# Optimization experiments

Measured on AMD Instinct MI355X. Metric: run time of the kernel, lower is better.

## Reference

```python
import jax, jax.numpy as jnp
import numpy as np
import math

NH, NKV, D = 32, 8, 128  # heads, kv heads, head dim

def _alibi_slopes(n):
    cp2 = 2 ** math.floor(math.log2(n))
    base = 2.0 ** (-8.0 / cp2)
    slopes = base ** np.arange(1, cp2 + 1, dtype=np.float32)
    if cp2 != n:
        extra_base = 2.0 ** (-4.0 / cp2)
        extra = extra_base ** np.arange(1, 1 + 2 * (n - cp2), 2, dtype=np.float32)
        slopes = np.concatenate([slopes, extra])
    return slopes.astype(np.float32)

def setup_inputs() -> dict:
    key = jax.random.key(0)
    k1, k2, k3 = jax.random.split(key, 3)
    B, S, H = 4, 1024, 4096
    qkv_out = NH * D + 2 * NKV * D  # 6144
    return {
        "hidden_states": jax.random.normal(k1, (B, S, H), jnp.float32) * 0.02,
        "w_qkv": jax.random.normal(k2, (H, qkv_out), jnp.float32) * 0.02,
        "w_o": jax.random.normal(k3, (NH * D, H), jnp.float32) * 0.02,
    }

def reference(hidden_states, w_qkv, w_o):
    B, S, H = hidden_states.shape
    G = NH // NKV  # query groups per kv head
    scale = D ** -0.5

    qkv = hidden_states @ w_qkv  # [B,S,6144]
    q = qkv[..., : NH * D].reshape(B, S, NKV, G, D)
    k = qkv[..., NH * D : NH * D + NKV * D].reshape(B, S, NKV, D)
    v = qkv[..., NH * D + NKV * D :].reshape(B, S, NKV, D)

    scores = jnp.einsum("bqhgd,bkhd->bhgqk", q, k) * scale  # [B,NKV,G,S,S]

    slopes = jnp.asarray(_alibi_slopes(NH)).reshape(NKV, G)  # head order
    pos = jnp.arange(S)
    rel = pos[:, None] - pos[None, :]  # i - j
    sqrt_dist = jnp.sqrt(jnp.maximum(rel, 0).astype(jnp.float32))
    bias = -slopes[:, :, None, None] * sqrt_dist  # ALiBi-sqrt bias
    bias = jnp.where(rel[None, None] >= 0, bias, -jnp.inf)  # causal mask

    attn = jax.nn.softmax(scores + bias[None], axis=-1)
    out = jnp.einsum("bhgqk,bkhd->bqhgd", attn, v).reshape(B, S, NH * D)
    return out @ w_o
```

## Files before the change

kernel.cpp:

```cpp
#include <hip/hip_runtime.h>
#include <stdint.h>

typedef __attribute__((ext_vector_type(4))) float floatx4;
typedef __attribute__((ext_vector_type(8))) short short8;
typedef unsigned short ushort_t;

#define DEVI __device__ __forceinline__

constexpr int Bc   = 4;
constexpr int Sc   = 1024;
constexpr int Hc   = 4096;
constexpr int NHc  = 32;
constexpr int NKVc = 8;
constexpr int Dc   = 128;
constexpr int QKVO = 6144;
constexpr int Mc   = Bc * Sc;

DEVI ushort_t f2bf(float f) {
  union { float f; unsigned u; } x; x.f = f;
  unsigned u = x.u;
  u += 0x7fffu + ((u >> 16) & 1u);
  return (ushort_t)(u >> 16);
}

DEVI short8 cvt8(floatx4 a, floatx4 b) {
  short8 r;
  r[0] = (short)f2bf(a[0]); r[1] = (short)f2bf(a[1]);
  r[2] = (short)f2bf(a[2]); r[3] = (short)f2bf(a[3]);
  r[4] = (short)f2bf(b[0]); r[5] = (short)f2bf(b[1]);
  r[6] = (short)f2bf(b[2]); r[7] = (short)f2bf(b[3]);
  return r;
}

DEVI void load_lds16(const ushort_t* g, ushort_t* l) {
  __builtin_amdgcn_global_load_lds(
      (const __attribute__((address_space(1))) void*)g,
      (__attribute__((address_space(3))) void*)l, 16, 0, 0);
}

#define BARRIER()  asm volatile("s_barrier" ::: "memory")
#define LGKM0()    asm volatile("s_waitcnt lgkmcnt(0)" ::: "memory")
#define VMCNT(n)   asm volatile("s_waitcnt vmcnt(" #n ")" ::: "memory")

__global__ __launch_bounds__(256)
void cvt_bf16(const float* __restrict__ src, ushort_t* __restrict__ dst, int n8)
{
  const int i = blockIdx.x * 256 + threadIdx.x;
  if (i >= n8) return;
  const floatx4 f0 = *(const floatx4*)(src + (size_t)i * 8);
  const floatx4 f1 = *(const floatx4*)(src + (size_t)i * 8 + 4);
  *(short8*)(dst + (size_t)i * 8) = cvt8(f0, f1);
}

__global__ __launch_bounds__(256)
void transpose_cvt(const float* __restrict__ src, ushort_t* __restrict__ dst,
                   int R, int C)
{
  __shared__ float ts[64][67];
  const int cb = C >> 6;
  const int r0 = (blockIdx.x / cb) << 6;
  const int c0 = (blockIdx.x % cb) << 6;
  const int t  = threadIdx.x;

  const int lr = t >> 4, lc = (t & 15) << 2;
#pragma unroll
  for (int i = 0; i < 4; ++i) {
    const floatx4 v = *(const floatx4*)(src + (size_t)(r0 + lr + 16 * i) * C + c0 + lc);
#pragma unroll
    for (int j = 0; j < 4; ++j) ts[lr + 16 * i][lc + j] = v[j];
  }
  __syncthreads();

  const int c     = ((t >> 6) << 4) + ((t & 63) >> 2);
  const int chunk = t & 3;
  short8 t0, t1;
#pragma unroll
  for (int k = 0; k < 8; ++k) t0[k] = (short)f2bf(ts[chunk * 16 + k][c]);
#pragma unroll
  for (int k = 0; k < 8; ++k) t1[k] = (short)f2bf(ts[chunk * 16 + 8 + k][c]);
  ushort_t* dp = dst + (size_t)(c0 + c) * R + r0 + chunk * 16;
  *(short8*)dp       = t0;
  *(short8*)(dp + 8) = t1;
}

__global__ __launch_bounds__(256)
void v_transpose(const ushort_t* __restrict__ qkv, ushort_t* __restrict__ vt)
{
  __shared__ ushort_t ts[64][72];
  const int bid = blockIdx.x;
  const int db  = bid & 1;
  const int sb  = (bid >> 1) & 15;
  const int hkv = (bid >> 5) & 7;
  const int b   = bid >> 8;
  const int t   = threadIdx.x;

  const ushort_t* src = qkv + (size_t)(b * Sc + sb * 64) * QKVO
                        + (NHc * Dc + NKVc * Dc) + hkv * Dc + db * 64;
  const int lr = t >> 3, lc = (t & 7) * 8;
  *(short8*)&ts[lr][lc]      = *(const short8*)(src + (size_t)lr * QKVO + lc);
  *(short8*)&ts[lr + 32][lc] = *(const short8*)(src + (size_t)(lr + 32) * QKVO + lc);
  __syncthreads();

  ushort_t* dst = vt + ((size_t)(b * NKVc + hkv) * Dc + db * 64) * Sc + sb * 64;
  const int dr  = t >> 2;
  const int sc0 = (t & 3) * 16;
  short8 o0, o1;
#pragma unroll
  for (int k = 0; k < 8; ++k) o0[k] = (short)ts[sc0 + k][dr];
#pragma unroll
  for (int k = 0; k < 8; ++k) o1[k] = (short)ts[sc0 + 8 + k][dr];
  *(short8*)(dst + (size_t)dr * Sc + sc0)     = o0;
  *(short8*)(dst + (size_t)dr * Sc + sc0 + 8) = o1;
}

template<int NFRAG, bool OBF16>
__global__ __launch_bounds__(512, 2)
void gemm_nt8d(const ushort_t* __restrict__ A, const ushort_t* __restrict__ BT,
               void* __restrict__ Cp, int M, int N, int K)
{
  constexpr int BN = 64 * NFRAG;
  __shared__ __align__(16) ushort_t As[2][256 * 64];
  __shared__ __align__(16) ushort_t Bs[2][BN * 64];

  const int nb  = N / BN;
  const int nwg = (M >> 8) * nb;
  int bid = blockIdx.x;
  bid = (bid & 7) * (nwg >> 3) + (bid >> 3);
  const int bm = bid / nb, bn = bid % nb;
  const int m0 = bm << 8, n0 = bn * BN;

  const int tid  = threadIdx.x;
  const int wid  = tid >> 6, lane = tid & 63;
  const int wm   = wid >> 2, wn = wid & 3;
  const int fr   = lane & 15;
  const int g16  = (lane >> 4) << 4;
  const int rsw  = (fr & 7) << 4;
  const int l8   = lane >> 3;
  const int scol = ((lane & 7) ^ l8) << 3;

  const int sr   = (wid << 3);
  const size_t Ks = (size_t)K;
  const ushort_t* agS = A  + (size_t)(m0 + sr + l8) * K + scol;
  const ushort_t* bgS = BT + (size_t)(n0 + sr + l8) * K + scol;

  const int rowA = (wm * 128 + fr) * 128;
  const int rowB = (wn * 16 * NFRAG + fr) * 128;
  const int cb0  = g16 ^ rsw;
  const int cb1  = (64 + g16) ^ rsw;

  const floatx4 fz = {0.f, 0.f, 0.f, 0.f};
  floatx4 acc[8][NFRAG];
#pragma unroll
  for (int i = 0; i < 8; ++i)
#pragma unroll
    for (int f = 0; f < NFRAG; ++f) acc[i][f] = fz;

  auto SAq0 = [&](int s, size_t kn) {
    load_lds16(agS + kn,            &As[s][(sr +   0) * 64]);
    load_lds16(agS + 128 * Ks + kn, &As[s][(sr + 128) * 64]);
  };
  auto SAq1 = [&](int s, size_t kn) {
    load_lds16(agS +  64 * Ks + kn, &As[s][(sr +  64) * 64]);
    load_lds16(agS + 192 * Ks + kn, &As[s][(sr + 192) * 64]);
  };
  auto SB01 = [&](int s, size_t kn) {
    load_lds16(bgS + kn,            &Bs[s][(sr +   0) * 64]);
    load_lds16(bgS +  64 * Ks + kn, &Bs[s][(sr +  64) * 64]);
  };
  auto SB2 = [&](int s, size_t kn) {
    load_lds16(bgS + 128 * Ks + kn, &Bs[s][(sr + 128) * 64]);
    if constexpr (NFRAG == 4)
      load_lds16(bgS + 192 * Ks + kn, &Bs[s][(sr + 192) * 64]);
  };

  SAq0(0, 0); SAq1(0, 0); SB01(0, 0); SB2(0, 0);
  SAq0(1, 64); SB01(1, 64); SB2(1, 64);
  VMCNT(0);
  BARRIER();

#define LDA(s, i, ks) (*(const short8*)((const char*)&As[s][0] + rowA + (i) * 2048 + ((ks) ? cb1 : cb0)))
#define LDB(s, f, ks) (*(const short8*)((const char*)&Bs[s][0] + rowB + (f) * 2048 + ((ks) ? cb1 : cb0)))

  const int NI = K >> 7;
  for (int it = 0; it < NI; ++it) {
    const size_t kt0 = (size_t)it << 7;
    const size_t k1 = kt0 + 64, k2 = kt0 + 128, k3 = kt0 + 192;
    const bool st2 = (it + 1 < NI);
    const bool st3 = st2;

    short8 aR[4], bR[NFRAG][2], bS[NFRAG][2];

#define MFMA_PH(base, barr, ks)                                              \
    __builtin_amdgcn_s_setprio(1);                                          \
    _Pragma("unroll")                                                       \
    for (int i = 0; i < 4; ++i)                                             \
      _Pragma("unroll")                                                     \
      for (int f = 0; f < NFRAG; ++f)                                       \
        acc[(base) + i][f] = __builtin_amdgcn_mfma_f32_16x16x32_bf16(       \
            aR[i], barr[f][ks], acc[(base) + i][f], 0, 0, 0);               \
    __builtin_amdgcn_s_setprio(0);

#pragma unroll
    for (int i = 0; i < 4; ++i) aR[i] = LDA(0, i, 0);
#pragma unroll
    for (int f = 0; f < NFRAG; ++f) { bR[f][0] = LDB(0, f, 0); bR[f][1] = LDB(0, f, 1); }
    SAq1(1, k1);
    VMCNT(4);
    BARRIER();
    LGKM0(); __builtin_amdgcn_sched_barrier(0);
    MFMA_PH(0, bR, 0)
    BARRIER();

#pragma unroll
    for (int i = 0; i < 4; ++i) aR[i] = LDA(1, i, 0);
#pragma unroll
    for (int f = 0; f < NFRAG; ++f) { bS[f][0] = LDB(1, f, 0); bS[f][1] = LDB(1, f, 1); }
    if (st2) SB01(0, k2);
    VMCNT(4);
    BARRIER();
    LGKM0(); __builtin_amdgcn_sched_barrier(0);
    MFMA_PH(0, bS, 0)
    BARRIER();

#pragma unroll
    for (int i = 0; i < 4; ++i) aR[i] = LDA(0, 4 + i, 0);
    if (st2) SB2(0, k2);
    if constexpr (NFRAG == 4) { VMCNT(4); } else { VMCNT(3); }
    BARRIER();
    LGKM0(); __builtin_amdgcn_sched_barrier(0);
    MFMA_PH(4, bR, 0)
    BARRIER();

#pragma unroll
    for (int i = 0; i < 4; ++i) aR[i] = LDA(1, 4 + i, 0);
    if (st3) SB01(1, k3);
    BARRIER();
    LGKM0(); __builtin_amdgcn_sched_barrier(0);
    MFMA_PH(4, bS, 0)
    BARRIER();

#pragma unroll
    for (int i = 0; i < 4; ++i) aR[i] = LDA(0, i, 1);
    if (st3) SB2(1, k3);
    BARRIER();
    LGKM0(); __builtin_amdgcn_sched_barrier(0);
    MFMA_PH(0, bR, 1)
    BARRIER();

#pragma unroll
    for (int i = 0; i < 4; ++i) aR[i] = LDA(1, i, 1);
    if (st2) SAq0(0, k2);
    BARRIER();
    LGKM0(); __builtin_amdgcn_sched_barrier(0);
    MFMA_PH(0, bS, 1)
    BARRIER();

#pragma unroll
    for (int i = 0; i < 4; ++i) aR[i] = LDA(0, 4 + i, 1);
    if (st3) SAq0(1, k3);
    BARRIER();
    LGKM0(); __builtin_amdgcn_sched_barrier(0);
    MFMA_PH(4, bR, 1)
    BARRIER();

#pragma unroll
    for (int i = 0; i < 4; ++i) aR[i] = LDA(1, 4 + i, 1);
    if (st2) SAq1(0, k2);
    VMCNT(4);
    BARRIER();
    LGKM0(); __builtin_amdgcn_sched_barrier(0);
    MFMA_PH(4, bS, 1)
    BARRIER();

#undef MFMA_PH
  }
#undef LDA
#undef LDB

  const int r4 = (lane >> 4) << 2;
#pragma unroll
  for (int i = 0; i < 8; ++i) {
#pragma unroll
    for (int rr = 0; rr < 4; ++rr) {
      const size_t row = (size_t)(m0 + wm * 128 + i * 16 + r4 + rr);
#pragma unroll
      for (int f = 0; f < NFRAG; ++f) {
        const size_t col = (size_t)(n0 + wn * 16 * NFRAG + f * 16 + fr);
        if constexpr (OBF16)
          ((ushort_t*)Cp)[row * N + col] = f2bf(acc[i][f][rr]);
        else
          ((float*)Cp)[row * N + col] = acc[i][f][rr];
      }
    }
  }
}

template<int NFRAG, bool OBF16>
__global__ __launch_bounds__(512, 2)
void gemm_nt8s(const ushort_t* __restrict__ A, const ushort_t* __restrict__ BT,
               void* __restrict__ Cp, int M, int N, int K)
{
  constexpr int BN = 64 * NFRAG;
  __shared__ __align__(16) ushort_t As[2][256 * 64];
  __shared__ __align__(16) ushort_t Bs[2][BN * 64];

  const int nb  = N / BN;
  const int nwg = (M >> 8) * nb;
  int bid = blockIdx.x;
  bid = (bid & 7) * (nwg >> 3) + (bid >> 3);
  const int bm = bid / nb, bn = bid % nb;
  const int m0 = bm << 8, n0 = bn * BN;

  const int tid  = threadIdx.x;
  const int wid  = tid >> 6, lane = tid & 63;
  const int wm   = wid >> 2, wn = wid & 3;
  const int fr   = lane & 15;
  const int g16  = (lane >> 4) << 4;
  const int rsw  = (fr & 7) << 4;
  const int l8   = lane >> 3;
  const int scol = ((lane & 7) ^ l8) << 3;

  const int sr   = (wid << 3);
  const size_t Ks = (size_t)K;
  const ushort_t* agS = A  + (size_t)(m0 + sr + l8) * K + scol;
  const ushort_t* bgS = BT + (size_t)(n0 + sr + l8) * K + scol;

  const int rowA = (wm * 128 + fr) * 128;
  const int rowB = (wn * 16 * NFRAG + fr) * 128;
  const int cb0  = g16 ^ rsw;
  const int cb1  = (64 + g16) ^ rsw;

  const floatx4 fz = {0.f, 0.f, 0.f, 0.f};
  floatx4 acc[8][NFRAG];
#pragma unroll
  for (int i = 0; i < 8; ++i)
#pragma unroll
    for (int f = 0; f < NFRAG; ++f) acc[i][f] = fz;

  auto SAq0 = [&](int s, size_t kn) {
    load_lds16(agS + kn,            &As[s][(sr +   0) * 64]);
    load_lds16(agS + 128 * Ks + kn, &As[s][(sr + 128) * 64]);
  };
  auto SAq1 = [&](int s, size_t kn) {
    load_lds16(agS +  64 * Ks + kn, &As[s][(sr +  64) * 64]);
    load_lds16(agS + 192 * Ks + kn, &As[s][(sr + 192) * 64]);
  };
  auto SB01 = [&](int s, size_t kn) {
    load_lds16(bgS + kn,            &Bs[s][(sr +   0) * 64]);
    load_lds16(bgS +  64 * Ks + kn, &Bs[s][(sr +  64) * 64]);
  };
  auto SB2 = [&](int s, size_t kn) {
    load_lds16(bgS + 128 * Ks + kn, &Bs[s][(sr + 128) * 64]);
    if constexpr (NFRAG == 4)
      load_lds16(bgS + 192 * Ks + kn, &Bs[s][(sr + 192) * 64]);
  };

  SAq0(0, 0); SAq1(0, 0); SB01(0, 0); SB2(0, 0);
  SB01(1, 64); SB2(1, 64);
  VMCNT(4);
  BARRIER();

#define LDA(s, i, ks) (*(const short8*)((const char*)&As[s][0] + rowA + (i) * 2048 + ((ks) ? cb1 : cb0)))
#define LDB(s, f, ks) (*(const short8*)((const char*)&Bs[s][0] + rowB + (f) * 2048 + ((ks) ? cb1 : cb0)))

  const int NI = K >> 7;
  for (int it = 0; it < NI; ++it) {
    const size_t kt0 = (size_t)it << 7;
    const size_t k1 = kt0 + 64, k2 = kt0 + 128, k3 = kt0 + 192;
    const bool st = (it + 1 < NI);

    short8 aR[4], bR[NFRAG][2];

#define MFMA_PH(base, ks)                                                    \
    __builtin_amdgcn_s_setprio(1);                                          \
    _Pragma("unroll")                                                       \
    for (int i = 0; i < 4; ++i)                                             \
      _Pragma("unroll")                                                     \
      for (int f = 0; f < NFRAG; ++f)                                       \
        acc[(base) + i][f] = __builtin_amdgcn_mfma_f32_16x16x32_bf16(       \
            aR[i], bR[f][ks], acc[(base) + i][f], 0, 0, 0);                 \
    __builtin_amdgcn_s_setprio(0);

#pragma unroll
    for (int i = 0; i < 4; ++i) aR[i] = LDA(0, i, 0);
#pragma unroll
    for (int f = 0; f < NFRAG; ++f) { bR[f][0] = LDB(0, f, 0); bR[f][1] = LDB(0, f, 1); }
    SAq0(1, k1);
    BARRIER();
    LGKM0(); __builtin_amdgcn_sched_barrier(0);
    MFMA_PH(0, 0)
    BARRIER();

#pragma unroll
    for (int i = 0; i < 4; ++i) aR[i] = LDA(0, 4 + i, 0);
    SAq1(1, k1);
    BARRIER();
    LGKM0(); __builtin_amdgcn_sched_barrier(0);
    MFMA_PH(4, 0)
    BARRIER();

#pragma unroll
    for (int i = 0; i < 4; ++i) aR[i] = LDA(0, i, 1);
    if (st) SB01(0, k2);
    BARRIER();
    LGKM0(); __builtin_amdgcn_sched_barrier(0);
    MFMA_PH(0, 1)
    BARRIER();

#pragma unroll
    for (int i = 0; i < 4; ++i) aR[i] = LDA(0, 4 + i, 1);
    if (st) { SB2(0, k2); VMCNT(4); } else { VMCNT(0); }
    BARRIER();
    LGKM0(); __builtin_amdgcn_sched_barrier(0);
    MFMA_PH(4, 1)
    BARRIER();

#pragma unroll
    for (int i = 0; i < 4; ++i) aR[i] = LDA(1, i, 0);
#pragma unroll
    for (int f = 0; f < NFRAG; ++f) { bR[f][0] = LDB(1, f, 0); bR[f][1] = LDB(1, f, 1); }
    if (st) SAq0(0, k2);
    BARRIER();
    LGKM0(); __builtin_amdgcn_sched_barrier(0);
    MFMA_PH(0, 0)
    BARRIER();

#pragma unroll
    for (int i = 0; i < 4; ++i) aR[i] = LDA(1, 4 + i, 0);
    if (st) SAq1(0, k2);
    BARRIER();
    LGKM0(); __builtin_amdgcn_sched_barrier(0);
    MFMA_PH(4, 0)
    BARRIER();

#pragma unroll
    for (int i = 0; i < 4; ++i) aR[i] = LDA(1, i, 1);
    if (st) SB01(1, k3);
    BARRIER();
    LGKM0(); __builtin_amdgcn_sched_barrier(0);
    MFMA_PH(0, 1)
    BARRIER();

#pragma unroll
    for (int i = 0; i < 4; ++i) aR[i] = LDA(1, 4 + i, 1);
    if (st) { SB2(1, k3); VMCNT(4); } else { VMCNT(0); }
    BARRIER();
    LGKM0(); __builtin_amdgcn_sched_barrier(0);
    MFMA_PH(4, 1)
    BARRIER();

#undef MFMA_PH
  }
#undef LDA
#undef LDB

  const int r4 = (lane >> 4) << 2;
#pragma unroll
  for (int i = 0; i < 8; ++i) {
#pragma unroll
    for (int rr = 0; rr < 4; ++rr) {
      const size_t row = (size_t)(m0 + wm * 128 + i * 16 + r4 + rr);
#pragma unroll
      for (int f = 0; f < NFRAG; ++f) {
        const size_t col = (size_t)(n0 + wn * 16 * NFRAG + f * 16 + fr);
        if constexpr (OBF16)
          ((ushort_t*)Cp)[row * N + col] = f2bf(acc[i][f][rr]);
        else
          ((float*)Cp)[row * N + col] = acc[i][f][rr];
      }
    }
  }
}

__global__ __launch_bounds__(256)
void attn_fwd(const ushort_t* __restrict__ qkv,
              const ushort_t* __restrict__ vt,
              ushort_t* __restrict__ attn)
{
  __shared__ __align__(16) ushort_t Plds[4][32 * 40];

  const int bid = blockIdx.x;
  const int x   = bid & 7;
  const int p   = bid >> 3;
  const int qb  = 31 - (p & 31);
  const int g   = ((p >> 5) << 3) + x;
  const int b   = g >> 3;
  const int hkv = g & 7;

  const int tid  = threadIdx.x;
  const int wid  = tid >> 6, lane = tid & 63;
  const int h    = hkv * 4 + wid;
  const int fr   = lane & 15;
  const int kk8  = (lane >> 4) << 3;
  const int q4   = (lane >> 4) << 2;
  const float slope = exp2f(-0.25f * (float)(h + 1));
  const float scale = 0.08838834764831845f;

  const ushort_t* qp  = qkv + (size_t)b * Sc * QKVO + (size_t)h * Dc;
  const ushort_t* kp  = qkv + (size_t)b * Sc * QKVO + NHc * Dc + (size_t)hkv * Dc;
  const ushort_t* vtp = vt + (size_t)(b * NKVc + hkv) * Dc * Sc;
  ushort_t* myP = &Plds[wid][0];

  const floatx4 fz = {0.f, 0.f, 0.f, 0.f};

  short8 qf[2][4];
#pragma unroll
  for (int t = 0; t < 2; ++t) {
    const int qrow = qb * 32 + t * 16 + fr;
#pragma unroll
    for (int s = 0; s < 4; ++s)
      qf[t][s] = *(const short8*)(qp + (size_t)qrow * QKVO + s * 32 + kk8);
  }

  floatx4 o[2][8];
#pragma unroll
  for (int t = 0; t < 2; ++t)
#pragma unroll
    for (int jj = 0; jj < 8; ++jj) o[t][jj] = fz;
  float mrow[2][4], lrow[2][4];
#pragma unroll
  for (int t = 0; t < 2; ++t)
#pragma unroll
    for (int rr = 0; rr < 4; ++rr) { mrow[t][rr] = -1e30f; lrow[t][rr] = 0.f; }

  for (int kb = 0; kb <= qb; ++kb) {
    floatx4 s_[2][2];
    s_[0][0] = fz; s_[0][1] = fz; s_[1][0] = fz; s_[1][1] = fz;
#pragma unroll
    for (int half = 0; half < 2; ++half) {
      const int kcol = kb * 32 + half * 16 + fr;
#pragma unroll
      for (int s = 0; s < 4; ++s) {
        const short8 kf = *(const short8*)(kp + (size_t)kcol * QKVO + s * 32 + kk8);
        s_[0][half] = __builtin_amdgcn_mfma_f32_16x16x32_bf16(qf[0][s], kf, s_[0][half], 0, 0, 0);
        s_[1][half] = __builtin_amdgcn_mfma_f32_16x16x32_bf16(qf[1][s], kf, s_[1][half], 0, 0, 0);
      }
    }

    short8 vf[8];
#pragma unroll
    for (int jj = 0; jj < 8; ++jj)
      vf[jj] = *(const short8*)(vtp + (size_t)(jj * 16 + fr) * Sc + kb * 32 + kk8);

#pragma unroll
    for (int t = 0; t < 2; ++t)
#pragma unroll
      for (int rr = 0; rr < 4; ++rr) {
        const int qg  = qb * 32 + t * 16 + q4 + rr;
        const int dk0 = qg - (kb * 32 + fr);
        const int dk1 = dk0 - 16;
        s_[t][0][rr] = (dk0 >= 0)
            ? s_[t][0][rr] * scale - slope * sqrtf((float)dk0) : -1e30f;
        s_[t][1][rr] = (dk1 >= 0)
            ? s_[t][1][rr] * scale - slope * sqrtf((float)dk1) : -1e30f;
      }

    float pmv[2][4];
#pragma unroll
    for (int t = 0; t < 2; ++t)
#pragma unroll
      for (int rr = 0; rr < 4; ++rr) {
        float pm = fmaxf(s_[t][0][rr], s_[t][1][rr]);
#pragma unroll
        for (int m = 1; m < 16; m <<= 1) pm = fmaxf(pm, __shfl_xor(pm, m));
        pmv[t][rr] = pm;
      }

    int need = 0;
#pragma unroll
    for (int t = 0; t < 2; ++t)
#pragma unroll
      for (int rr = 0; rr < 4; ++rr)
        need |= (pmv[t][rr] > mrow[t][rr] + 8.f) ? 1 : 0;
    if (__any(need)) {
#pragma unroll
      for (int t = 0; t < 2; ++t)
#pragma unroll
        for (int rr = 0; rr < 4; ++rr) {
          const float mnew = fmaxf(mrow[t][rr], pmv[t][rr]);
          const float corr = __expf(mrow[t][rr] - mnew);
          lrow[t][rr] *= corr;
          mrow[t][rr] = mnew;
#pragma unroll
          for (int jj = 0; jj < 8; ++jj) o[t][jj][rr] *= corr;
        }
    }

#pragma unroll
    for (int t = 0; t < 2; ++t)
#pragma unroll
      for (int rr = 0; rr < 4; ++rr) {
        const float p0 = __expf(s_[t][0][rr] - mrow[t][rr]);
        const float p1 = __expf(s_[t][1][rr] - mrow[t][rr]);
        lrow[t][rr] += p0 + p1;
        myP[(t * 16 + q4 + rr) * 40 + fr]      = f2bf(p0);
        myP[(t * 16 + q4 + rr) * 40 + 16 + fr] = f2bf(p1);
      }
    short8 pa[2];
    pa[0] = *(const short8*)&myP[fr * 40 + kk8];
    pa[1] = *(const short8*)&myP[(16 + fr) * 40 + kk8];

#pragma unroll
    for (int jj = 0; jj < 8; ++jj) {
      o[0][jj] = __builtin_amdgcn_mfma_f32_16x16x32_bf16(pa[0], vf[jj], o[0][jj], 0, 0, 0);
      o[1][jj] = __builtin_amdgcn_mfma_f32_16x16x32_bf16(pa[1], vf[jj], o[1][jj], 0, 0, 0);
    }
  }

#pragma unroll
  for (int t = 0; t < 2; ++t)
#pragma unroll
    for (int rr = 0; rr < 4; ++rr) {
      float rs = lrow[t][rr];
#pragma unroll
      for (int m = 1; m < 16; m <<= 1) rs += __shfl_xor(rs, m);
      const float inv = 1.f / rs;
      const size_t tok = (size_t)b * Sc + qb * 32 + t * 16 + q4 + rr;
#pragma unroll
      for (int jj = 0; jj < 8; ++jj)
        attn[tok * (size_t)(NHc * Dc) + h * Dc + jj * 16 + fr] = f2bf(o[t][jj][rr] * inv);
    }
}

extern "C" void kernel_launch(void* const* d_in, const int* in_sizes, int n_in,
                              void* d_out, int out_size, void* d_ws, size_t ws_size,
                              hipStream_t stream)
{
  const float* hidden = (const float*)d_in[0];
  const float* w_qkv  = (const float*)d_in[1];
  const float* w_o    = (const float*)d_in[2];
  float* out = (float*)d_out;

  ushort_t* wqT   = (ushort_t*)d_ws;
  ushort_t* hidb  = wqT + (size_t)QKVO * Hc;
  ushort_t* qkvb  = hidb + (size_t)Mc * Hc;
  ushort_t* attnb = hidb;
  ushort_t* woT   = wqT;
  ushort_t* vtb   = wqT + (size_t)Mc * Hc;

  cvt_bf16<<<dim3((Mc * Hc / 8) / 256), dim3(256), 0, stream>>>(
      hidden, hidb, Mc * Hc / 8);
  transpose_cvt<<<dim3((Hc / 64) * (QKVO / 64)), dim3(256), 0, stream>>>(
      w_qkv, wqT, Hc, QKVO);
  gemm_nt8d<3, true><<<dim3((Mc / 256) * (QKVO / 192)), dim3(512), 0, stream>>>(
      hidb, wqT, qkvb, Mc, QKVO, Hc);
  v_transpose<<<dim3(1024), dim3(256), 0, stream>>>(qkvb, vtb);
  attn_fwd<<<dim3(1024), dim3(256), 0, stream>>>(qkvb, vtb, attnb);
  transpose_cvt<<<dim3((Hc / 64) * (Hc / 64)), dim3(256), 0, stream>>>(
      w_o, woT, Hc, Hc);
  gemm_nt8s<4, false><<<dim3((Mc / 256) * (Hc / 256)), dim3(512), 0, stream>>>(
      attnb, woT, out, Mc, Hc, Hc);
}
```

Before: 682.7 us.

## Balance causal attention work by pairing complementary 16-row query tiles per block

Each attention block now handles two 16-row query tiles (63-j and j) one after the other, instead of a single 32-row tile. Every block therefore gets a roughly equal number of causal key blocks, which removes the load imbalance of the triangular mask. The cost is that K/V tiles are no longer shared across 32 query rows per load, so global K/V traffic per MFMA rises. The tiles are also processed serially, which halves the accumulator registers and may improve occupancy.

```diff
diff --git a/kernel.cpp b/kernel.cpp
--- a/kernel.cpp
+++ b/kernel.cpp
@@ -477,12 +477,12 @@
               const ushort_t* __restrict__ vt,
               ushort_t* __restrict__ attn)
 {
-  __shared__ __align__(16) ushort_t Plds[4][32 * 40];
+  __shared__ __align__(16) ushort_t Plds[4][16 * 40];
 
   const int bid = blockIdx.x;
   const int x   = bid & 7;
   const int p   = bid >> 3;
-  const int qb  = 31 - (p & 31);
+  const int j   = p & 31;
   const int g   = ((p >> 5) << 3) + x;
   const int b   = g >> 3;
   const int hkv = g & 7;
@@ -503,123 +503,105 @@
 
   const floatx4 fz = {0.f, 0.f, 0.f, 0.f};
 
-  short8 qf[2][4];
-#pragma unroll
-  for (int t = 0; t < 2; ++t) {
-    const int qrow = qb * 32 + t * 16 + fr;
+  auto process = [&](const int qb16) {
+    short8 qf[4];
+    const int qrow = qb16 * 16 + fr;
 #pragma unroll
     for (int s = 0; s < 4; ++s)
-      qf[t][s] = *(const short8*)(qp + (size_t)qrow * QKVO + s * 32 + kk8);
-  }
-
-  floatx4 o[2][8];
-#pragma unroll
-  for (int t = 0; t < 2; ++t)
-#pragma unroll
-    for (int jj = 0; jj < 8; ++jj) o[t][jj] = fz;
-  float mrow[2][4], lrow[2][4];
-#pragma unroll
-  for (int t = 0; t < 2; ++t)
-#pragma unroll
-    for (int rr = 0; rr < 4; ++rr) { mrow[t][rr] = -1e30f; lrow[t][rr] = 0.f; }
-
-  for (int kb = 0; kb <= qb; ++kb) {
-    floatx4 s_[2][2];
-    s_[0][0] = fz; s_[0][1] = fz; s_[1][0] = fz; s_[1][1] = fz;
-#pragma unroll
-    for (int half = 0; half < 2; ++half) {
-      const int kcol = kb * 32 + half * 16 + fr;
-#pragma unroll
-      for (int s = 0; s < 4; ++s) {
-        const short8 kf = *(const short8*)(kp + (size_t)kcol * QKVO + s * 32 + kk8);
-        s_[0][half] = __builtin_amdgcn_mfma_f32_16x16x32_bf16(qf[0][s], kf, s_[0][half], 0, 0, 0);
-        s_[1][half] = __builtin_amdgcn_mfma_f32_16x16x32_bf16(qf[1][s], kf, s_[1][half], 0, 0, 0);
+      qf[s] = *(const short8*)(qp + (size_t)qrow * QKVO + s * 32 + kk8);
+
+    floatx4 o[8];
+#pragma unroll
+    for (int jj = 0; jj < 8; ++jj) o[jj] = fz;
+    float mrow[4], lrow[4];
+#pragma unroll
+    for (int rr = 0; rr < 4; ++rr) { mrow[rr] = -1e30f; lrow[rr] = 0.f; }
+
+    const int kbmax = qb16 >> 1;
+    for (int kb = 0; kb <= kbmax; ++kb) {
+      floatx4 s_[2];
+      s_[0] = fz; s_[1] = fz;
+#pragma unroll
+      for (int half = 0; half < 2; ++half) {
+        const int kcol = kb * 32 + half * 16 + fr;
+#pragma unroll
+        for (int s = 0; s < 4; ++s) {
+          const short8 kf = *(const short8*)(kp + (size_t)kcol * QKVO + s * 32 + kk8);
+          s_[half] = __builtin_amdgcn_mfma_f32_16x16x32_bf16(qf[s], kf, s_[half], 0, 0, 0);
+        }
       }
-    }
-
-    short8 vf[8];
-#pragma unroll
-    for (int jj = 0; jj < 8; ++jj)
-      vf[jj] = *(const short8*)(vtp + (size_t)(jj * 16 + fr) * Sc + kb * 32 + kk8);
-
-#pragma unroll
-    for (int t = 0; t < 2; ++t)
+
+      short8 vf[8];
+#pragma unroll
+      for (int jj = 0; jj < 8; ++jj)
+        vf[jj] = *(const short8*)(vtp + (size_t)(jj * 16 + fr) * Sc + kb * 32 + kk8);
+
 #pragma unroll
       for (int rr = 0; rr < 4; ++rr) {
-        const int qg  = qb * 32 + t * 16 + q4 + rr;
+        const int qg  = qb16 * 16 + q4 + rr;
         const int dk0 = qg - (kb * 32 + fr);
         const int dk1 = dk0 - 16;
-        s_[t][0][rr] = (dk0 >= 0)
-            ? s_[t][0][rr] * scale - slope * sqrtf((float)dk0) : -1e30f;
-        s_[t][1][rr] = (dk1 >= 0)
-            ? s_[t][1][rr] * scale - slope * sqrtf((float)dk1) : -1e30f;
+        s_[0][rr] = (dk0 >= 0)
+            ? s_[0][rr] * scale - slope * sqrtf((float)dk0) : -1e30f;
+        s_[1][rr] = (dk1 >= 0)
+            ? s_[1][rr] * scale - slope * sqrtf((float)dk1) : -1e30f;
       }
 
-    float pmv[2][4];
-#pragma unroll
-    for (int t = 0; t < 2; ++t)
+      float pmv[4];
 #pragma unroll
       for (int rr = 0; rr < 4; ++rr) {
-        float pm = fmaxf(s_[t][0][rr], s_[t][1][rr]);
+        float pm = fmaxf(s_[0][rr], s_[1][rr]);
 #pragma unroll
         for (int m = 1; m < 16; m <<= 1) pm = fmaxf(pm, __shfl_xor(pm, m));
-        pmv[t][rr] = pm;
+        pmv[rr] = pm;
       }
 
-    int need = 0;
-#pragma unroll
-    for (int t = 0; t < 2; ++t)
+      int need = 0;
 #pragma unroll
       for (int rr = 0; rr < 4; ++rr)
-        need |= (pmv[t][rr] > mrow[t][rr] + 8.f) ? 1 : 0;
-    if (__any(need)) {
-#pragma unroll
-      for (int t = 0; t < 2; ++t)
+        need |= (pmv[rr] > mrow[rr] + 8.f) ? 1 : 0;
+      if (__any(need)) {
 #pragma unroll
         for (int rr = 0; rr < 4; ++rr) {
-          const float mnew = fmaxf(mrow[t][rr], pmv[t][rr]);
-          const float corr = __expf(mrow[t][rr] - mnew);
-          lrow[t][rr] *= corr;
-          mrow[t][rr] = mnew;
-#pragma unroll
-          for (int jj = 0; jj < 8; ++jj) o[t][jj][rr] *= corr;
+          const float mnew = fmaxf(mrow[rr], pmv[rr]);
+          const float corr = __expf(mrow[rr] - mnew);
+          lrow[rr] *= corr;
+          mrow[rr] = mnew;
+#pragma unroll
+          for (int jj = 0; jj < 8; ++jj) o[jj][rr] *= corr;
         }
+      }
+
+#pragma unroll
+      for (int rr = 0; rr < 4; ++rr) {
+        const float p0 = __expf(s_[0][rr] - mrow[rr]);
+        const float p1 = __expf(s_[1][rr] - mrow[rr]);
+        lrow[rr] += p0 + p1;
+        myP[(q4 + rr) * 40 + fr]      = f2bf(p0);
+        myP[(q4 + rr) * 40 + 16 + fr] = f2bf(p1);
+      }
+      const short8 pa = *(const short8*)&myP[fr * 40 + kk8];
+
+#pragma unroll
+      for (int jj = 0; jj < 8; ++jj)
+        o[jj] = __builtin_amdgcn_mfma_f32_16x16x32_bf16(pa, vf[jj], o[jj], 0, 0, 0);
     }
 
 #pragma unroll
-    for (int t = 0; t < 2; ++t)
-#pragma unroll
-      for (int rr = 0; rr < 4; ++rr) {
-        const float p0 = __expf(s_[t][0][rr] - mrow[t][rr]);
-        const float p1 = __expf(s_[t][1][rr] - mrow[t][rr]);
-        lrow[t][rr] += p0 + p1;
-        myP[(t * 16 + q4 + rr) * 40 + fr]      = f2bf(p0);
-        myP[(t * 16 + q4 + rr) * 40 + 16 + fr] = f2bf(p1);
-      }
-    short8 pa[2];
-    pa[0] = *(const short8*)&myP[fr * 40 + kk8];
-    pa[1] = *(const short8*)&myP[(16 + fr) * 40 + kk8];
-
-#pragma unroll
-    for (int jj = 0; jj < 8; ++jj) {
-      o[0][jj] = __builtin_amdgcn_mfma_f32_16x16x32_bf16(pa[0], vf[jj], o[0][jj], 0, 0, 0);
-      o[1][jj] = __builtin_amdgcn_mfma_f32_16x16x32_bf16(pa[1], vf[jj], o[1][jj], 0, 0, 0);
-    }
-  }
-
-#pragma unroll
-  for (int t = 0; t < 2; ++t)
-#pragma unroll
     for (int rr = 0; rr < 4; ++rr) {
-      float rs = lrow[t][rr];
+      float rs = lrow[rr];
 #pragma unroll
       for (int m = 1; m < 16; m <<= 1) rs += __shfl_xor(rs, m);
       const float inv = 1.f / rs;
-      const size_t tok = (size_t)b * Sc + qb * 32 + t * 16 + q4 + rr;
+      const size_t tok = (size_t)b * Sc + qb16 * 16 + q4 + rr;
 #pragma unroll
       for (int jj = 0; jj < 8; ++jj)
-        attn[tok * (size_t)(NHc * Dc) + h * Dc + jj * 16 + fr] = f2bf(o[t][jj][rr] * inv);
+        attn[tok * (size_t)(NHc * Dc) + h * Dc + jj * 16 + fr] = f2bf(o[jj][rr] * inv);
     }
+  };
+
+  process(63 - j);
+  process(j);
 }
 
 extern "C" void kernel_launch(void* const* d_in, const int* in_sizes, int n_in,
```

Result: slower. 715.5 us (+4.8%).
